# Kernel optimization log

Measured on AMD Instinct MI355X. Metric: run time of the kernel, lower is better.

The kernel has to match this reference:

```python
import jax, jax.numpy as jnp
import numpy as np

PATCH = 3      # patch_size = (3, 3)
STRIDE = 1     # filter_patch_stride == compare_stride == 1
EPS = 1e-12    # F.normalize eps


def extract_patches(x, ph, pw, stride):
    """x: (B, C, H, W) -> (B, nH*nW, C, ph, pw), valid patches."""
    B, C, H, W = x.shape
    oh = (H - ph) // stride + 1
    ow = (W - pw) // stride + 1
    rows = (jnp.arange(oh) * stride)[:, None] + jnp.arange(ph)[None, :]  # (oh, ph)
    cols = (jnp.arange(ow) * stride)[:, None] + jnp.arange(pw)[None, :]  # (ow, pw)
    # gather -> (B, C, oh, ph, ow, pw)
    p = x[:, :, rows[:, :, None, None], cols[None, None, :, :]]
    return p.transpose(0, 2, 4, 1, 3, 5).reshape(B, oh * ow, C, ph, pw)


def l2norm(x, axis):
    # matches F.normalize(p=2): x / max(||x||, eps)
    return x / jnp.maximum(jnp.linalg.norm(x, axis=axis, keepdims=True), EPS)


def setup_inputs() -> dict:
    key = jax.random.key(0)
    k1, k2 = jax.random.split(key)
    pred_style = jax.random.normal(k1, (4, 256, 64, 64), dtype=jnp.float32)
    target_style = jax.random.normal(k2, (4, 256, 64, 64), dtype=jnp.float32)
    return {"pred_style": pred_style, "target_style": target_style}


def reference(pred_style, target_style):
    # patches of the raw (unnormalized) features
    tp = extract_patches(target_style, PATCH, PATCH, STRIDE)   # (B, nP, C, ph, pw)
    pp = extract_patches(pred_style, PATCH, PATCH, STRIDE)     # (B, nP, C, ph, pw)

    # best_match: normalize content feature over channels, style patches over channel dim (dim=2)
    x1n = l2norm(pred_style, axis=1)
    tpn = l2norm(tp, axis=2)
    x1p = extract_patches(x1n, PATCH, PATCH, STRIDE)           # (B, nP, C, ph, pw)

    # conv-as-cosine-correlation == batched patch dot products, then argmax over style patches
    scores = jnp.einsum('bqcij,bpcij->bqp', x1p, tpn)          # (B, nP, nP)
    match = jnp.argmax(scores, axis=2)                         # (B, nP)

    # gather best-matching target patches (indices detached in original via .data)
    new_t = jnp.take_along_axis(tp, match[:, :, None, None, None], axis=1)
    return jnp.mean((pp - new_t) ** 2)
```

## Files before the change

kernel.cpp:

```cpp
#include <hip/hip_runtime.h>
#include <hip/hip_bf16.h>

#define NB 4
#define CH 256
#define HH 64
#define WW 64
#define NPIX 4096
#define OH 62
#define NPATCH 3844
#define KDIM 256
#define EPSN 1e-12f
#define VROW 68
#define SEG 8
#define PST 68

typedef __attribute__((ext_vector_type(8))) short short8;
typedef __attribute__((ext_vector_type(4))) float f32x4;

__device__ __forceinline__ float bf16_to_f32(unsigned short u) {
    return __uint_as_float((unsigned)u << 16);
}
__device__ __forceinline__ unsigned short f32_to_bf16(float f) {
    __hip_bfloat16 h = __float2bfloat16(f);
    return *(unsigned short*)&h;
}

__global__ __launch_bounds__(256) void k_prep(const float* __restrict__ pred,
                                              const float* __restrict__ tgt,
                                              __hip_bfloat16* __restrict__ Xn,
                                              __hip_bfloat16* __restrict__ Tn,
                                              float* __restrict__ ssP, float* __restrict__ invP,
                                              float* __restrict__ ssT, float* __restrict__ invT,
                                              unsigned long long* __restrict__ keys,
                                              float* __restrict__ out) {
    const int bz = blockIdx.y;
    const int b = bz >> 1, which = bz & 1;
    const float* src = (which ? tgt : pred) + (size_t)b * CH * NPIX;
    unsigned short* dst = (unsigned short*)((which ? Tn : Xn) + (size_t)b * NPIX * CH);
    float* ss_g  = (which ? ssT  : ssP)  + b * NPIX;
    float* inv_g = (which ? invT : invP) + b * NPIX;
    const int pix0 = blockIdx.x * 64;
    const int t = threadIdx.x, lane = t & 63, wv = t >> 6;

    int gid = (bz * 64 + blockIdx.x) * 256 + t;
    if (gid < NB * NPATCH) keys[gid] = 0ull;
    if (gid == 0) out[0] = 0.f;

    __shared__ unsigned short stage[CH][PST];
    __shared__ float partial[16][68];
    __shared__ float inv_s[64];

    const int cb = t >> 4, chk = t & 15;
    float ss0 = 0.f, ss1 = 0.f, ss2 = 0.f, ss3 = 0.f;
#pragma unroll
    for (int r = 0; r < 16; ++r) {
        int c = cb * 16 + r;
        float4 v = *(const float4*)&src[(size_t)c * NPIX + pix0 + chk * 4];
        ss0 += v.x * v.x; ss1 += v.y * v.y; ss2 += v.z * v.z; ss3 += v.w * v.w;
        ushort4 sv;
        sv.x = f32_to_bf16(v.x); sv.y = f32_to_bf16(v.y);
        sv.z = f32_to_bf16(v.z); sv.w = f32_to_bf16(v.w);
        *(ushort4*)&stage[c][chk * 4] = sv;
    }
    float4 pv; pv.x = ss0; pv.y = ss1; pv.z = ss2; pv.w = ss3;
    *(float4*)&partial[cb][chk * 4] = pv;
    __syncthreads();
    if (t < 64) {
        float ss = 0.f;
#pragma unroll
        for (int r = 0; r < 16; ++r) ss += partial[r][t];
        float inv = 1.f / fmaxf(sqrtf(ss), EPSN);
        ss_g[pix0 + t] = ss;
        inv_g[pix0 + t] = inv;
        inv_s[t] = inv;
    }
    __syncthreads();
    for (int p = wv; p < 64; p += 4) {
        float iv = inv_s[p];
#pragma unroll
        for (int cc = 0; cc < 4; ++cc) {
            int c = cc * 64 + lane;
            float v = bf16_to_f32(stage[c][p]) * iv;
            dst[(size_t)(pix0 + p) * CH + c] = f32_to_bf16(v);
        }
    }
}

__device__ __forceinline__ void gload_lds16(const void* g, void* l) {
    __builtin_amdgcn_global_load_lds(
        (const __attribute__((address_space(1))) void*)g,
        (__attribute__((address_space(3))) void*)l, 16, 0, 0);
}

__global__ __launch_bounds__(256, 2) void k_gemm(const __hip_bfloat16* __restrict__ A,
                                                 const __hip_bfloat16* __restrict__ Bm,
                                                 unsigned short* __restrict__ Dout) {
    __shared__ __align__(16) short smem[32768];
#define ASOFF(buf) ((buf) * 8192)
#define BSOFF(buf) (16384 + (buf) * 8192)

    const int t = threadIdx.x;
    const int lane = t & 63, wv = t >> 6;
    const int wm = wv >> 1, wn = wv & 1;

    const int bid = ((blockIdx.z << 5) + blockIdx.y) * 32 + blockIdx.x;
    const int swz = ((bid & 7) << 9) + (bid >> 3);
    const int z = swz >> 10, by = (swz >> 5) & 31, bx = swz & 31;

    const int row0 = by * 128, col0 = bx * 128;
    const short* Ag = (const short*)A + (size_t)z * NPIX * CH;
    const short* Bg = (const short*)Bm + (size_t)z * NPIX * CH;
    unsigned short* D = Dout + (size_t)z * NPIX * NPIX;

    const int srow = t >> 3;
    const int kce  = ((t & 7) ^ (srow & 7)) * 8;

    f32x4 acc[4][4] = {};

#define STAGE_K(buf, k0)                                                                   \
    do {                                                                                   \
        _Pragma("unroll")                                                                  \
        for (int rr_ = 0; rr_ < 4; ++rr_)                                                  \
            gload_lds16(Ag + (size_t)(row0 + rr_ * 32 + srow) * KDIM + (k0) + kce,         \
                        &smem[ASOFF(buf) + rr_ * 2048 + wv * 512]);                        \
        _Pragma("unroll")                                                                  \
        for (int rr_ = 0; rr_ < 4; ++rr_)                                                  \
            gload_lds16(Bg + (size_t)(col0 + rr_ * 32 + srow) * KDIM + (k0) + kce,         \
                        &smem[BSOFF(buf) + rr_ * 2048 + wv * 512]);                        \
    } while (0)

    const int rsel = lane & 15, kq = lane >> 4;
    const int rx = rsel & 7;

#define CONSUME(buf)                                                                       \
    do {                                                                                   \
        _Pragma("unroll")                                                                  \
        for (int s = 0; s < 2; ++s) {                                                      \
            const int pk = (((s << 2) + kq) ^ rx) * 8;                                     \
            short8 a_[4], b_[4];                                                           \
            _Pragma("unroll")                                                              \
            for (int mi = 0; mi < 4; ++mi)                                                 \
                a_[mi] = *(const short8*)&smem[ASOFF(buf) + (wm * 64 + mi * 16 + rsel) * 64 + pk]; \
            _Pragma("unroll")                                                              \
            for (int ni = 0; ni < 4; ++ni)                                                 \
                b_[ni] = *(const short8*)&smem[BSOFF(buf) + (wn * 64 + ni * 16 + rsel) * 64 + pk]; \
            _Pragma("unroll")                                                              \
            for (int mi = 0; mi < 4; ++mi)                                                 \
                _Pragma("unroll")                                                          \
                for (int ni = 0; ni < 4; ++ni)                                             \
                    acc[mi][ni] = __builtin_amdgcn_mfma_f32_16x16x32_bf16(a_[mi], b_[ni],  \
                                                                          acc[mi][ni], 0, 0, 0); \
        }                                                                                  \
    } while (0)

#define KITER(it, VMC)                                              \
    do {                                                            \
        asm volatile("s_waitcnt vmcnt(" #VMC ")" ::: "memory");     \
        __builtin_amdgcn_sched_barrier(0);                          \
        __builtin_amdgcn_s_barrier();                               \
        __builtin_amdgcn_sched_barrier(0);                          \
        CONSUME((it) & 1);                                          \
        asm volatile("s_waitcnt lgkmcnt(0)" ::: "memory");          \
        __builtin_amdgcn_sched_barrier(0);                          \
        __builtin_amdgcn_s_barrier();                               \
        __builtin_amdgcn_sched_barrier(0);                          \
        if ((it) < 2) STAGE_K((it) & 1, ((it) + 2) * 64);           \
    } while (0)

    STAGE_K(0, 0);
    STAGE_K(1, 64);
    KITER(0, 8);
    KITER(1, 8);
    KITER(2, 8);
    KITER(3, 0);
#undef KITER
#undef CONSUME
#undef STAGE_K

    const int rbase = (lane >> 4) * 4, cbase = lane & 15;
    unsigned short* Cs = (unsigned short*)smem;
#pragma unroll
    for (int mi = 0; mi < 4; ++mi)
#pragma unroll
        for (int ni = 0; ni < 4; ++ni) {
            int c = wn * 64 + ni * 16 + cbase;
#pragma unroll
            for (int r = 0; r < 4; ++r) {
                int row = wm * 64 + mi * 16 + rbase + r;
                int pc = (((c >> 3) ^ (row & 15)) * 8) + (c & 7);
                Cs[row * 128 + pc] = f32_to_bf16(acc[mi][ni][r]);
            }
        }
    __syncthreads();
#pragma unroll
    for (int rd = 0; rd < 8; ++rd) {
        int rr = rd * 16 + (t >> 4);
        int pc = ((t & 15) ^ (rr & 15)) * 8;
        uint4 v = *(const uint4*)&Cs[rr * 128 + pc];
        *(uint4*)&D[(size_t)(row0 + rr) * NPIX + col0 + (t & 15) * 8] = v;
    }
#undef ASOFF
#undef BSOFF
}

__device__ __forceinline__ void load_tile16(const unsigned short* __restrict__ D,
                                            int row, int col, float* f) {
    const unsigned short* rp = D + (size_t)row * NPIX + col;
    uint4 u0 = *(const uint4*)rp;
    uint4 u1 = *(const uint4*)(rp + 8);
    const unsigned* w0 = (const unsigned*)&u0;
    const unsigned* w1 = (const unsigned*)&u1;
#pragma unroll
    for (int w = 0; w < 4; ++w) {
        f[2 * w]         = bf16_to_f32((unsigned short)w0[w]);
        f[2 * w + 1]     = bf16_to_f32((unsigned short)(w0[w] >> 16));
        f[8 + 2 * w]     = bf16_to_f32((unsigned short)w1[w]);
        f[8 + 2 * w + 1] = bf16_to_f32((unsigned short)(w1[w] >> 16));
    }
}

__global__ __launch_bounds__(256) void k_score(const unsigned short* __restrict__ Dbase,
                                               unsigned long long* __restrict__ keys) {
    const int z = blockIdx.z;
    const unsigned short* D = Dbase + (size_t)z * NPIX * NPIX;
    const int t = threadIdx.x;

    const int d = (int)blockIdx.x - 61;
    const int adg = d < 0 ? -d : d;
    const int len = 62 - adg;
    const int s0 = blockIdx.y * SEG;
    if (s0 >= len) return;
    const int steps = min(SEG, len - s0);
    const int qr0 = (d > 0 ? d : 0) + s0;
    const int pr0 = qr0 - d;

    __shared__ __align__(16) float V[64 * VROW];

    const int a = t >> 2, b0 = (t & 3) * 16;
    const int g = t >> 6, qc = t & 63;
    const int qcr = qc < OH ? qc : (OH - 1);
    const int pc0 = g * 16;
    const int kmax = (g == 3) ? 14 : 16;

    float A[16], B[16], C[16];
    load_tile16(D, (qr0 + 0) * 64 + a, (pr0 + 0) * 64 + b0, A);
    load_tile16(D, (qr0 + 1) * 64 + a, (pr0 + 1) * 64 + b0, B);

    for (int k = 0; k < steps; ++k) {
        load_tile16(D, (qr0 + k + 2) * 64 + a, (pr0 + k + 2) * 64 + b0, C);
        float v[16];
#pragma unroll
        for (int e = 0; e < 16; ++e) v[e] = A[e] + B[e] + C[e];
        if (k) __syncthreads();
#pragma unroll
        for (int e = 0; e < 16; e += 4)
            *(f32x4*)&V[a * VROW + b0 + e] = *(const f32x4*)&v[e];
        __syncthreads();

        float r0[16], r1[20], r2[20];
#pragma unroll
        for (int e = 0; e < 16; e += 4)
            *(f32x4*)&r0[e] = *(const f32x4*)&V[qcr * VROW + pc0 + e];
#pragma unroll
        for (int e = 0; e < 20; e += 4)
            *(f32x4*)&r1[e] = *(const f32x4*)&V[(qcr + 1) * VROW + pc0 + e];
#pragma unroll
        for (int e = 0; e < 20; e += 4)
            *(f32x4*)&r2[e] = *(const f32x4*)&V[(qcr + 2) * VROW + pc0 + e];
        float best = -1e30f; int bpc = 0;
#pragma unroll
        for (int kk = 0; kk < 16; ++kk) {
            float s = r0[kk] + r1[kk + 1] + r2[kk + 2];
            if (kk < kmax && s > best) { best = s; bpc = pc0 + kk; }
        }
        if (qc < OH) {
            unsigned u = __float_as_uint(best);
            u = (best >= 0.f) ? (u | 0x80000000u) : ~u;
            unsigned long long key = ((unsigned long long)u << 12)
                                   | (unsigned)((63 - (pr0 + k)) << 6)
                                   | (unsigned)(63 - bpc);
            atomicMax(&keys[(size_t)z * NPATCH + (qr0 + k) * OH + qc], key);
        }
#pragma unroll
        for (int e = 0; e < 16; ++e) { A[e] = B[e]; B[e] = C[e]; }
    }
}

__global__ void k_loss(const unsigned short* __restrict__ Dbase,
                       const unsigned long long* __restrict__ keys,
                       const float* __restrict__ ssPb, const float* __restrict__ invPb,
                       const float* __restrict__ ssTb, const float* __restrict__ invTb,
                       float* __restrict__ out) {
    const int z = blockIdx.y;
    const unsigned short* D = Dbase + (size_t)z * NPIX * NPIX;
    const float* ssP  = ssPb  + z * NPIX;
    const float* invP = invPb + z * NPIX;
    const float* ssT  = ssTb  + z * NPIX;
    const float* invT = invTb + z * NPIX;
    int q = blockIdx.x * 256 + threadIdx.x;
    float acc = 0.f;
    if (q < NPATCH) {
        int qr = q / OH, qc = q - qr * OH;
        int qpix = qr * WW + qc;
        unsigned long long key = keys[(size_t)z * NPATCH + q];
        int mpr = 63 - (int)((key >> 6) & 63);
        int mpc = 63 - (int)(key & 63);
        int mpix = mpr * WW + mpc;
#pragma unroll
        for (int i = 0; i < 3; ++i)
#pragma unroll
            for (int j = 0; j < 3; ++j) {
                int off = i * WW + j;
                int y = qpix + off, x = mpix + off;
                float Dv = bf16_to_f32(D[(size_t)y * NPIX + x]);
                float nP = ssP[y] * invP[y];
                float nT = ssT[x] * invT[x];
                acc += ssP[y] + ssT[x] - 2.f * Dv * nP * nT;
            }
    }
#pragma unroll
    for (int s = 32; s > 0; s >>= 1) acc += __shfl_down(acc, s, 64);
    if ((threadIdx.x & 63) == 0)
        atomicAdd(out, acc * (1.f / 35426304.f));
}

extern "C" void kernel_launch(void* const* d_in, const int* in_sizes, int n_in,
                              void* d_out, int out_size, void* d_ws, size_t ws_size,
                              hipStream_t stream) {
    const float* pred = (const float*)d_in[0];
    const float* tgt  = (const float*)d_in[1];
    char* ws = (char*)d_ws;
    unsigned short*     Dws  = (unsigned short*)(ws);
    __hip_bfloat16*     Xn   = (__hip_bfloat16*)(ws + 134217728);
    __hip_bfloat16*     Tn   = (__hip_bfloat16*)(ws + 142606336);
    float*              ssP  = (float*)(ws + 150994944);
    float*              invP = (float*)(ws + 151060480);
    float*              ssT  = (float*)(ws + 151126016);
    float*              invT = (float*)(ws + 151191552);
    unsigned long long* keys = (unsigned long long*)(ws + 151257088);

    k_prep<<<dim3(64, 8), 256, 0, stream>>>(pred, tgt, Xn, Tn, ssP, invP, ssT, invT,
                                            keys, (float*)d_out);
    k_gemm<<<dim3(32, 32, 4), 256, 0, stream>>>(Xn, Tn, Dws);
    k_score<<<dim3(123, 8, 4), 256, 0, stream>>>(Dws, keys);
    k_loss<<<dim3(16, 4), 256, 0, stream>>>(Dws, keys, ssP, invP, ssT, invT,
                                            (float*)d_out);
}
```

Measured before the change: 181.2 us.

## Enlarge GEMM block tile to 256x256 with 512 threads and direct stores

```diff
diff --git a/kernel.cpp b/kernel.cpp
--- a/kernel.cpp
+++ b/kernel.cpp
@@ -92,22 +92,22 @@
         (__attribute__((address_space(3))) void*)l, 16, 0, 0);
 }
 
-__global__ __launch_bounds__(256, 2) void k_gemm(const __hip_bfloat16* __restrict__ A,
+__global__ __launch_bounds__(512, 2) void k_gemm(const __hip_bfloat16* __restrict__ A,
                                                  const __hip_bfloat16* __restrict__ Bm,
                                                  unsigned short* __restrict__ Dout) {
-    __shared__ __align__(16) short smem[32768];
-#define ASOFF(buf) ((buf) * 8192)
-#define BSOFF(buf) (16384 + (buf) * 8192)
+    __shared__ __align__(16) short smem[65536];
+#define ASOFF(buf) ((buf) * 16384)
+#define BSOFF(buf) (32768 + (buf) * 16384)
 
     const int t = threadIdx.x;
     const int lane = t & 63, wv = t >> 6;
-    const int wm = wv >> 1, wn = wv & 1;
-
-    const int bid = ((blockIdx.z << 5) + blockIdx.y) * 32 + blockIdx.x;
-    const int swz = ((bid & 7) << 9) + (bid >> 3);
-    const int z = swz >> 10, by = (swz >> 5) & 31, bx = swz & 31;
-
-    const int row0 = by * 128, col0 = bx * 128;
+    const int wm = wv >> 2, wn = wv & 3;
+
+    const int bid = ((blockIdx.z << 4) + blockIdx.y) * 16 + blockIdx.x;
+    const int swz = ((bid & 7) << 7) + (bid >> 3);
+    const int z = swz >> 8, by = (swz >> 4) & 15, bx = swz & 15;
+
+    const int row0 = by * 256, col0 = bx * 256;
     const short* Ag = (const short*)A + (size_t)z * NPIX * CH;
     const short* Bg = (const short*)Bm + (size_t)z * NPIX * CH;
     unsigned short* D = Dout + (size_t)z * NPIX * NPIX;
@@ -115,18 +115,18 @@
     const int srow = t >> 3;
     const int kce  = ((t & 7) ^ (srow & 7)) * 8;
 
-    f32x4 acc[4][4] = {};
+    f32x4 acc[8][4] = {};
 
 #define STAGE_K(buf, k0)                                                                   \
     do {                                                                                   \
         _Pragma("unroll")                                                                  \
         for (int rr_ = 0; rr_ < 4; ++rr_)                                                  \
-            gload_lds16(Ag + (size_t)(row0 + rr_ * 32 + srow) * KDIM + (k0) + kce,         \
-                        &smem[ASOFF(buf) + rr_ * 2048 + wv * 512]);                        \
+            gload_lds16(Ag + (size_t)(row0 + rr_ * 64 + srow) * KDIM + (k0) + kce,         \
+                        &smem[ASOFF(buf) + rr_ * 4096 + wv * 512]);                        \
         _Pragma("unroll")                                                                  \
         for (int rr_ = 0; rr_ < 4; ++rr_)                                                  \
-            gload_lds16(Bg + (size_t)(col0 + rr_ * 32 + srow) * KDIM + (k0) + kce,         \
-                        &smem[BSOFF(buf) + rr_ * 2048 + wv * 512]);                        \
+            gload_lds16(Bg + (size_t)(col0 + rr_ * 64 + srow) * KDIM + (k0) + kce,         \
+                        &smem[BSOFF(buf) + rr_ * 4096 + wv * 512]);                        \
     } while (0)
 
     const int rsel = lane & 15, kq = lane >> 4;
@@ -137,67 +137,74 @@
         _Pragma("unroll")                                                                  \
         for (int s = 0; s < 2; ++s) {                                                      \
             const int pk = (((s << 2) + kq) ^ rx) * 8;                                     \
-            short8 a_[4], b_[4];                                                           \
+            short8 a_[8], b_[4];                                                           \
             _Pragma("unroll")                                                              \
-            for (int mi = 0; mi < 4; ++mi)                                                 \
-                a_[mi] = *(const short8*)&smem[ASOFF(buf) + (wm * 64 + mi * 16 + rsel) * 64 + pk]; \
+            for (int mi = 0; mi < 8; ++mi)                                                 \
+                a_[mi] = *(const short8*)&smem[ASOFF(buf) + (wm * 128 + mi * 16 + rsel) * 64 + pk]; \
             _Pragma("unroll")                                                              \
             for (int ni = 0; ni < 4; ++ni)                                                 \
-                b_[ni] = *(const short8*)&smem[BSOFF(buf) + (wn * 64 + ni * 16 + rsel) * 64 + pk]; \
+                b_[ni] = *(const short8*)&smem[BSOFF(buf) + (wn * 64 + ni * 16 + rsel) * 64 + pk];  \
             _Pragma("unroll")                                                              \
-            for (int mi = 0; mi < 4; ++mi)                                                 \
+            for (int mi = 0; mi < 8; ++mi)                                                 \
                 _Pragma("unroll")                                                          \
                 for (int ni = 0; ni < 4; ++ni)                                             \
-                    acc[mi][ni] = __builtin_amdgcn_mfma_f32_16x16x32_bf16(a_[mi], b_[ni],  \
+                    acc[mi][ni] = __builtin_amdgcn_mfma_f32_16x16x32_bf16(b_[ni], a_[mi],  \
                                                                           acc[mi][ni], 0, 0, 0); \
         }                                                                                  \
     } while (0)
 
-#define KITER(it, VMC)                                              \
+#define WAIT_VM(N)                                                  \
     do {                                                            \
-        asm volatile("s_waitcnt vmcnt(" #VMC ")" ::: "memory");     \
+        asm volatile("s_waitcnt vmcnt(" #N ")" ::: "memory");       \
         __builtin_amdgcn_sched_barrier(0);                          \
         __builtin_amdgcn_s_barrier();                               \
         __builtin_amdgcn_sched_barrier(0);                          \
-        CONSUME((it) & 1);                                          \
+    } while (0)
+
+#define WAIT_LGKM_BAR()                                             \
+    do {                                                            \
         asm volatile("s_waitcnt lgkmcnt(0)" ::: "memory");          \
         __builtin_amdgcn_sched_barrier(0);                          \
         __builtin_amdgcn_s_barrier();                               \
         __builtin_amdgcn_sched_barrier(0);                          \
-        if ((it) < 2) STAGE_K((it) & 1, ((it) + 2) * 64);           \
     } while (0)
 
     STAGE_K(0, 0);
     STAGE_K(1, 64);
-    KITER(0, 8);
-    KITER(1, 8);
-    KITER(2, 8);
-    KITER(3, 0);
-#undef KITER
+
+    WAIT_VM(8);
+    CONSUME(0);
+    WAIT_LGKM_BAR();
+    STAGE_K(0, 128);
+
+    WAIT_VM(8);
+    CONSUME(1);
+    WAIT_LGKM_BAR();
+    STAGE_K(1, 192);
+
+    WAIT_VM(8);
+    CONSUME(0);
+
+    WAIT_VM(0);
+    CONSUME(1);
+#undef WAIT_LGKM_BAR
+#undef WAIT_VM
 #undef CONSUME
 #undef STAGE_K
 
-    const int rbase = (lane >> 4) * 4, cbase = lane & 15;
-    unsigned short* Cs = (unsigned short*)smem;
-#pragma unroll
-    for (int mi = 0; mi < 4; ++mi)
+    const int r16 = lane & 15, c4 = (lane >> 4) * 4;
+#pragma unroll
+    for (int mi = 0; mi < 8; ++mi) {
+        const size_t rowoff = (size_t)(row0 + wm * 128 + mi * 16 + r16) * NPIX;
 #pragma unroll
         for (int ni = 0; ni < 4; ++ni) {
-            int c = wn * 64 + ni * 16 + cbase;
-#pragma unroll
-            for (int r = 0; r < 4; ++r) {
-                int row = wm * 64 + mi * 16 + rbase + r;
-                int pc = (((c >> 3) ^ (row & 15)) * 8) + (c & 7);
-                Cs[row * 128 + pc] = f32_to_bf16(acc[mi][ni][r]);
-            }
+            uint2 u;
+            u.x = (unsigned)f32_to_bf16(acc[mi][ni][0]) |
+                  ((unsigned)f32_to_bf16(acc[mi][ni][1]) << 16);
+            u.y = (unsigned)f32_to_bf16(acc[mi][ni][2]) |
+                  ((unsigned)f32_to_bf16(acc[mi][ni][3]) << 16);
+            *(uint2*)&D[rowoff + col0 + wn * 64 + ni * 16 + c4] = u;
         }
-    __syncthreads();
-#pragma unroll
-    for (int rd = 0; rd < 8; ++rd) {
-        int rr = rd * 16 + (t >> 4);
-        int pc = ((t & 15) ^ (rr & 15)) * 8;
-        uint4 v = *(const uint4*)&Cs[rr * 128 + pc];
-        *(uint4*)&D[(size_t)(row0 + rr) * NPIX + col0 + (t & 15) * 8] = v;
     }
 #undef ASOFF
 #undef BSOFF
@@ -341,7 +348,7 @@
 
     k_prep<<<dim3(64, 8), 256, 0, stream>>>(pred, tgt, Xn, Tn, ssP, invP, ssT, invT,
                                             keys, (float*)d_out);
-    k_gemm<<<dim3(32, 32, 4), 256, 0, stream>>>(Xn, Tn, Dws);
+    k_gemm<<<dim3(16, 16, 4), 512, 0, stream>>>(Xn, Tn, Dws);
     k_score<<<dim3(123, 8, 4), 256, 0, stream>>>(Dws, keys);
     k_loss<<<dim3(16, 4), 256, 0, stream>>>(Dws, keys, ssP, invP, ssT, invT,
                                             (float*)d_out);
```

Measured after the change: 186.5 us. +2.9%, slower.
